# Optimization experiments

Hardware: AMD Instinct MI355X
Metric: run time of the kernel (lower is better)

## Reference

```python
import jax, jax.numpy as jnp
import numpy as np

GRID_SIZE, SPLINE_ORDER = 5, 3  # efficient-kan KANLinear defaults
NUM_BASES = GRID_SIZE + SPLINE_ORDER


def b_splines(x, grid):
    # x: (N, in_dim), grid: (in_dim, GRID_SIZE + 2*SPLINE_ORDER + 1)
    xe = x[..., None]
    bases = ((xe >= grid[:, :-1]) & (xe < grid[:, 1:])).astype(x.dtype)
    for k in range(1, SPLINE_ORDER + 1):  # Cox-de Boor recursion (static, 3 iters)
        left = (xe - grid[:, : -(k + 1)]) / (grid[:, k:-1] - grid[:, : -(k + 1)])
        right = (grid[:, k + 1:] - xe) / (grid[:, k + 1:] - grid[:, 1:-k])
        bases = left * bases[..., :-1] + right * bases[..., 1:]
    return bases  # (N, in_dim, NUM_BASES)


def kan_linear(x, grid, base_w, spline_w, scaler):
    # base branch: SiLU(x) @ W_base^T ; spline branch: B-spline basis @ scaled spline weights
    n = x.shape[0]
    out_dim = base_w.shape[0]
    base = jax.nn.silu(x) @ base_w.T
    bs = b_splines(x, grid).reshape(n, -1)                    # (N, in*NUM_BASES)
    sw = (spline_w * scaler[..., None]).reshape(out_dim, -1)  # (out, in*NUM_BASES)
    return base + bs @ sw.T


def setup_inputs() -> dict:
    key = jax.random.key(0)
    N, E, F, H, C, L = 50000, 500000, 128, 128, 40, 3
    ks = jax.random.split(key, 8)
    x = jax.random.normal(ks[0], (N, F), dtype=jnp.float32)
    edge_index = jax.random.randint(ks[1], (2, E), 0, N)
    # KAN grid (registered buffer in efficient-kan): uniform over [-1,1] extended by spline_order
    h_step = 2.0 / GRID_SIZE
    pts = np.arange(-SPLINE_ORDER, GRID_SIZE + SPLINE_ORDER + 1) * h_step - 1.0
    grid_mp = jnp.asarray(np.tile(pts, (F, 1)), dtype=jnp.float32)
    D = F + L * H  # skip-concat dim into output KANLinear
    grid_out = jnp.asarray(np.tile(pts, (D, 1)), dtype=jnp.float32)
    s = 0.1
    conv_base_w = jax.random.normal(ks[2], (L, H, F), dtype=jnp.float32) * s
    conv_spline_w = jax.random.normal(ks[3], (L, H, F, NUM_BASES), dtype=jnp.float32) * s
    conv_scaler = jnp.ones((L, H, F), dtype=jnp.float32)
    conv_bias = jnp.zeros((L, H), dtype=jnp.float32)
    bn_gamma = jnp.ones((L, H), dtype=jnp.float32)
    bn_beta = jnp.zeros((L, H), dtype=jnp.float32)
    out_base_w = jax.random.normal(ks[4], (C, D), dtype=jnp.float32) * s
    out_spline_w = jax.random.normal(ks[5], (C, D, NUM_BASES), dtype=jnp.float32) * s
    out_scaler = jnp.ones((C, D), dtype=jnp.float32)
    return dict(x=x, edge_index=edge_index, grid_mp=grid_mp, conv_base_w=conv_base_w,
                conv_spline_w=conv_spline_w, conv_scaler=conv_scaler, conv_bias=conv_bias,
                bn_gamma=bn_gamma, bn_beta=bn_beta, grid_out=grid_out,
                out_base_w=out_base_w, out_spline_w=out_spline_w, out_scaler=out_scaler)


def reference(x, edge_index, grid_mp, conv_base_w, conv_spline_w, conv_scaler, conv_bias,
              bn_gamma, bn_beta, grid_out, out_base_w, out_spline_w, out_scaler):
    N = x.shape[0]
    L = conv_base_w.shape[0]
    # GCN normalization with self-loops (computed once; identical each layer)
    loop = jnp.arange(N)
    src = jnp.concatenate([edge_index[0], loop])
    dst = jnp.concatenate([edge_index[1], loop])
    deg = jax.ops.segment_sum(jnp.ones_like(src, dtype=x.dtype), dst, num_segments=N)
    dinv = jnp.where(deg > 0, jax.lax.rsqrt(jnp.maximum(deg, 1.0)), 0.0)
    norm = dinv[src] * dinv[dst]  # (E+N,)
    feats = [x]
    for i in range(L):  # static layer loop
        h = kan_linear(x, grid_mp, conv_base_w[i], conv_spline_w[i], conv_scaler[i])
        # symmetric-normalized sparse aggregation (gather on src, scatter-add on dst)
        h = jax.ops.segment_sum(h[src] * norm[:, None], dst, num_segments=N) + conv_bias[i]
        # BatchNorm1d (training mode: biased batch statistics over nodes)
        mu = h.mean(axis=0)
        var = h.var(axis=0)
        x = (h - mu) * jax.lax.rsqrt(var + 1e-5) * bn_gamma[i] + bn_beta[i]
        feats.append(x)  # dropout p=0.0 is identity
    xc = jnp.concatenate(feats, axis=1)  # skip-concat: (N, F + L*H)
    logits = kan_linear(xc, grid_out, out_base_w, out_spline_w, out_scaler)
    return jax.nn.log_softmax(logits, axis=1)
```

## Files before the change

kernel.cpp:

```cpp
#include <hip/hip_runtime.h>
#include <hip/hip_bf16.h>
#include <math.h>

#define F_IN   128
#define HID    128
#define NLAYER 3
#define NCLS   40
#define DCAT   512
#define OOUT   64

typedef short s16x8 __attribute__((ext_vector_type(8)));
typedef unsigned short u16x8 __attribute__((ext_vector_type(8)));
typedef unsigned short u16x4 __attribute__((ext_vector_type(4)));
typedef float f32x4 __attribute__((ext_vector_type(4)));


static __device__ __forceinline__ float silu_f(float x) {
    return x / (1.f + __expf(-x));
}

static __device__ __forceinline__ unsigned short f2bf_rn(float f) {
    union { __hip_bfloat16 h; unsigned short u; } cv;
    cv.h = __float2bfloat16(f);
    return cv.u;
}

static __device__ __forceinline__ void gload_lds16(const void* g, void* l) {
    __builtin_amdgcn_global_load_lds(
        (const __attribute__((address_space(1))) void*)g,
        (__attribute__((address_space(3))) void*)l, 16, 0, 0);
}


__global__ __launch_bounds__(256) void deg_init_kernel(int* deg, int N) {
    for (int i = blockIdx.x * blockDim.x + threadIdx.x; i < N; i += gridDim.x * blockDim.x)
        deg[i] = 1;
}

__global__ __launch_bounds__(256) void deg_count_kernel(const int* __restrict__ dst, int E, int* deg) {
    for (int i = blockIdx.x * blockDim.x + threadIdx.x; i < E; i += gridDim.x * blockDim.x)
        atomicAdd(&deg[dst[i]], 1);
}

__global__ __launch_bounds__(256) void dinv_kernel(const int* __restrict__ deg, float* dinv, int N) {
    for (int i = blockIdx.x * blockDim.x + threadIdx.x; i < N; i += gridDim.x * blockDim.x)
        dinv[i] = rsqrtf((float)deg[i]);
}

__global__ __launch_bounds__(256) void scan_reduce_kernel(const int* __restrict__ deg, int* __restrict__ bsum, int N) {
    __shared__ int sh[256];
    int t = threadIdx.x;
    int e = blockIdx.x * 256 + t;
    sh[t] = (e < N) ? deg[e] : 0;
    __syncthreads();
#pragma unroll
    for (int off = 128; off > 0; off >>= 1) {
        if (t < off) sh[t] += sh[t + off];
        __syncthreads();
    }
    if (t == 0) bsum[blockIdx.x] = sh[0];
}

__global__ __launch_bounds__(256) void scan_top_kernel(const int* __restrict__ bsum, int* __restrict__ bbase, int nsb) {
    __shared__ int sh[256];
    int t = threadIdx.x;
    int chunk = (nsb + 255) >> 8;
    int begin = t * chunk;
    int end = begin + chunk; if (end > nsb) end = nsb;
    int s = 0;
    for (int i = begin; i < end; ++i) s += bsum[i];
    sh[t] = s;
    __syncthreads();
#pragma unroll
    for (int off = 1; off < 256; off <<= 1) {
        int v = 0;
        if (t >= off) v = sh[t - off];
        __syncthreads();
        if (t >= off) sh[t] += v;
        __syncthreads();
    }
    int run = (t == 0) ? 0 : sh[t - 1];
    for (int i = begin; i < end; ++i) {
        bbase[i] = run;
        run += bsum[i];
    }
}

__global__ __launch_bounds__(256) void scan_write_kernel(const int* __restrict__ deg,
                                                         const int* __restrict__ bbase,
                                                         int* __restrict__ offs, int* __restrict__ cursor, int N) {
    __shared__ int sh[256];
    int t = threadIdx.x;
    int e = blockIdx.x * 256 + t;
    int d = (e < N) ? deg[e] : 0;
    sh[t] = d;
    __syncthreads();
#pragma unroll
    for (int off = 1; off < 256; off <<= 1) {
        int v = 0;
        if (t >= off) v = sh[t - off];
        __syncthreads();
        if (t >= off) sh[t] += v;
        __syncthreads();
    }
    int incl = sh[t] + bbase[blockIdx.x];
    int excl = incl - d;
    if (e < N) {
        offs[e] = excl;
        cursor[e] = excl;
        if (e == N - 1) offs[N] = incl;
    }
}

__global__ __launch_bounds__(256) void fill_kernel(const int* __restrict__ src, const int* __restrict__ dst,
                                                   int E, int N, int* cursor, int* __restrict__ csr) {
    int total = E + N;
    for (int i = blockIdx.x * blockDim.x + threadIdx.x; i < total; i += gridDim.x * blockDim.x) {
        if (i < E) {
            int d = dst[i];
            int p = atomicAdd(&cursor[d], 1);
            csr[p] = src[i];
        } else {
            int n = i - E;
            int p = atomicAdd(&cursor[n], 1);
            csr[p] = n;
        }
    }
}

__global__ __launch_bounds__(256) void pack_conv_mfma(const float* __restrict__ bw,
                                                      const float* __restrict__ sw,
                                                      const float* __restrict__ sc,
                                                      unsigned short* __restrict__ wpk) {
    int total = NLAYER * 9 * 128 * 128;
    for (int idx = blockIdx.x * blockDim.x + threadIdx.x; idx < total; idx += gridDim.x * blockDim.x) {
        int kd = idx & 127;
        int o  = (idx >> 7) & 127;
        int cc = (idx >> 14) % 9;
        int l  = idx / (9 << 14);
        int k = kd ^ ((o & 7) << 3);
        float v;
        if (cc == 8) {
            v = bw[(l * 128 + o) * 128 + k];
        } else {
            int f = cc * 16 + (k >> 3);
            int j = k & 7;
            int base = (l * 128 + o) * 128 + f;
            v = sw[base * 8 + j] * sc[base];
        }
        wpk[idx] = f2bf_rn(v);
    }
}

__global__ __launch_bounds__(256) void pack_out_mfma(const float* __restrict__ bw,
                                                     const float* __restrict__ sw,
                                                     const float* __restrict__ sc,
                                                     unsigned short* __restrict__ wpk) {
    int total = 4 * 9 * 64 * 128;
    for (int idx = blockIdx.x * blockDim.x + threadIdx.x; idx < total; idx += gridDim.x * blockDim.x) {
        int kd = idx & 127;
        int o  = (idx >> 7) & 63;
        int cc = (idx >> 13) % 9;
        int g  = idx / (9 << 13);
        int k = kd ^ ((o & 7) << 3);
        float v = 0.f;
        if (o < NCLS) {
            if (cc == 8) {
                int f = g * 128 + k;
                v = bw[o * DCAT + f];
            } else {
                int f = g * 128 + cc * 16 + (k >> 3);
                int j = k & 7;
                int base = o * DCAT + f;
                v = sw[base * 8 + j] * sc[base];
            }
        }
        wpk[idx] = f2bf_rn(v);
    }
}


__global__ __launch_bounds__(256) void copyx_kernel(const float* __restrict__ x, float* __restrict__ xc, int N) {
    int total = N * F_IN;
    for (int idx = blockIdx.x * blockDim.x + threadIdx.x; idx < total; idx += gridDim.x * blockDim.x) {
        int n = idx >> 7, f = idx & 127;
        xc[(size_t)n * DCAT + f] = x[idx];
    }
}

__global__ __launch_bounds__(512) void affine_init_kernel(float* scA, float* shA) {
    int i = threadIdx.x;
    scA[i] = 1.f; shA[i] = 0.f;
}

template<bool CONV, bool INIT>
__global__ __launch_bounds__(256, 2) void kan_fused_kernel(
    const float* __restrict__ xc, int in_off,
    const float* __restrict__ scA, const float* __restrict__ shA,
    const unsigned short* __restrict__ wconv,
    const unsigned short* __restrict__ wout,
    unsigned short* __restrict__ silbuf,
    unsigned short* __restrict__ htmp,
    const float* __restrict__ dinv,
    float* __restrict__ out_acc, int N) {

    constexpr int LDS_WC = CONV ? 32768 : 0;
    __shared__ __align__(16) char lds[32768 + LDS_WC + 16384];
    char* lds_phi = lds;
    char* lds_wc  = lds + 32768;
    char* lds_wo  = lds + 32768 + LDS_WC;

    const int tid = threadIdx.x;
    const int lane = tid & 63;
    const int wave = tid >> 6;
    const int wr = wave >> 1, wc = wave & 1;
    const int l15 = lane & 15, lg = lane >> 4;
    const int nblk = blockIdx.x * 128;

    const float g0 = -1.f - 3.f * 0.4f;
    const float invh = 1.f / 0.4f;

    const int fg = tid & 3;
    const int n0 = tid >> 2;

    f32x4 accc[4][4];
    f32x4 acco[4][2];
    if (CONV) {
#pragma unroll
        for (int r = 0; r < 4; ++r)
#pragma unroll
            for (int c = 0; c < 4; ++c) accc[r][c] = (f32x4)0.f;
    }
#pragma unroll
    for (int r = 0; r < 4; ++r)
#pragma unroll
        for (int c = 0; c < 2; ++c) acco[r][c] = (f32x4)0.f;

    float4 xq[2], scq, shq;
    auto ldx = [&](int cc) {
        int f0 = in_off + cc * 16 + fg * 4;
        scq = *(const float4*)(scA + f0);
        shq = *(const float4*)(shA + f0);
        int gn0 = nblk + n0, gn1 = gn0 + 64;
        xq[0] = (gn0 < N) ? *(const float4*)(xc + (size_t)gn0 * DCAT + f0) : (float4){0.f,0.f,0.f,0.f};
        xq[1] = (gn1 < N) ? *(const float4*)(xc + (size_t)gn1 * DCAT + f0) : (float4){0.f,0.f,0.f,0.f};
    };

    u16x8 pcur[2][4];
    auto phi_compute = [&](int ccc) {
#pragma unroll
        for (int g2 = 0; g2 < 2; ++g2) {
            float xi[4] = {xq[g2].x, xq[g2].y, xq[g2].z, xq[g2].w};
            float scr[4] = {scq.x, scq.y, scq.z, scq.w};
            float shr[4] = {shq.x, shq.y, shq.z, shq.w};
            u16x4 sv;
#pragma unroll
            for (int fl = 0; fl < 4; ++fl) {
                float y = fmaf(xi[fl], scr[fl], shr[fl]);
                sv[fl] = f2bf_rn(silu_f(y));
                float t = (y - g0) * invh;
                float cf = floorf(t);
                int c = (int)cf;
                float u = t - cf;
                float um = 1.f - u;
                float u2 = u * u;
                float um2 = um * um;
                float w0 = um2 * um * (1.f / 6.f);
                float w3 = u2 * u * (1.f / 6.f);
                float w1 = fmaf(fmaf(0.5f, u, -1.f), u2, 2.f / 3.f);
                float w2 = fmaf(fmaf(-0.5f, u, 0.5f), u2, fmaf(0.5f, u, 1.f / 6.f));
                bool e[11];
#pragma unroll
                for (int v = 0; v < 11; ++v) e[v] = (c == v);
#pragma unroll
                for (int s = 0; s < 8; ++s) {
                    float val = 0.f;
                    val = e[s] ? w3 : val;
                    val = e[s + 1] ? w2 : val;
                    val = e[s + 2] ? w1 : val;
                    val = e[s + 3] ? w0 : val;
                    pcur[g2][fl][s] = f2bf_rn(val);
                }
            }
            int gn = nblk + n0 + g2 * 64;
            if (gn < N) {
                int fdst = (ccc * 16 + fg * 4) ^ ((n0 & 7) << 3);
                *(u16x4*)(silbuf + (size_t)gn * 128 + fdst) = sv;
            }
        }
    };

    auto stage_w = [&](int cc) {
        if (CONV) {
            const unsigned short* wcsrc = wconv + (size_t)cc * 128 * 128;
#pragma unroll
            for (int i = 0; i < 8; ++i) {
                int e = tid + i * 256;
                gload_lds16(wcsrc + e * 8, lds_wc + e * 16);
            }
        }
        const unsigned short* wosrc = wout + (size_t)cc * 64 * 128;
#pragma unroll
        for (int i = 0; i < 4; ++i) {
            int e = tid + i * 256;
            gload_lds16(wosrc + e * 8, lds_wo + e * 16);
        }
    };

    auto mfma_phase = [&]() {
#pragma unroll
        for (int kk = 0; kk < 4; ++kk) {
            const int kb = kk * 64 + lg * 16;
            s16x8 af[4];
#pragma unroll
            for (int r = 0; r < 4; ++r) {
                int n = wr * 64 + r * 16 + l15;
                af[r] = *(const s16x8*)(lds_phi + n * 256 + (kb ^ ((n & 7) << 4)));
            }
            if (CONV) {
#pragma unroll
                for (int c = 0; c < 4; ++c) {
                    int o = wc * 64 + c * 16 + l15;
                    s16x8 b = *(const s16x8*)(lds_wc + o * 256 + (kb ^ ((o & 7) << 4)));
#pragma unroll
                    for (int r = 0; r < 4; ++r)
                        accc[r][c] = __builtin_amdgcn_mfma_f32_16x16x32_bf16(af[r], b, accc[r][c], 0, 0, 0);
                }
            }
#pragma unroll
            for (int c = 0; c < 2; ++c) {
                int o = wc * 32 + c * 16 + l15;
                s16x8 b = *(const s16x8*)(lds_wo + o * 256 + (kb ^ ((o & 7) << 4)));
#pragma unroll
                for (int r = 0; r < 4; ++r)
                    acco[r][c] = __builtin_amdgcn_mfma_f32_16x16x32_bf16(af[r], b, acco[r][c], 0, 0, 0);
            }
        }
    };

    ldx(0);
    phi_compute(0);

    for (int cc = 0; cc < 8; ++cc) {
        __syncthreads();
        stage_w(cc);
#pragma unroll
        for (int g2 = 0; g2 < 2; ++g2) {
            int n = n0 + g2 * 64;
            int swz = (n & 7) << 4;
#pragma unroll
            for (int i = 0; i < 4; ++i) {
                int byte = n * 256 + ((fg * 64 + i * 16) ^ swz);
                *(u16x8*)(lds_phi + byte) = pcur[g2][i];
            }
        }
        __syncthreads();
        if (cc < 7) ldx(cc + 1);
        mfma_phase();
        if (cc < 7) phi_compute(cc + 1);
    }

    __syncthreads();
    stage_w(8);
    {
        const unsigned short* ssrc = silbuf + (size_t)nblk * 128;
#pragma unroll
        for (int i = 0; i < 8; ++i) {
            int e = tid + i * 256;
            gload_lds16(ssrc + e * 8, lds_phi + e * 16);
        }
    }
    __syncthreads();
    mfma_phase();

#pragma unroll
    for (int r = 0; r < 4; ++r) {
        int nb = nblk + wr * 64 + r * 16 + lg * 4;
        if (CONV) {
#pragma unroll
            for (int c = 0; c < 4; ++c) {
                int o = wc * 64 + c * 16 + l15;
#pragma unroll
                for (int q = 0; q < 4; ++q) {
                    int n = nb + q;
                    if (n < N) htmp[(size_t)n * HID + o] = f2bf_rn(accc[r][c][q] * dinv[n]);
                }
            }
        }
#pragma unroll
        for (int c = 0; c < 2; ++c) {
            int o = wc * 32 + c * 16 + l15;
#pragma unroll
            for (int q = 0; q < 4; ++q) {
                int n = nb + q;
                if (n < N) {
                    size_t a = (size_t)n * OOUT + o;
                    float v = acco[r][c][q];
                    if (!INIT) v += out_acc[a];
                    out_acc[a] = v;
                }
            }
        }
    }
}

__global__ __launch_bounds__(256) void agg_kernel(const unsigned short* __restrict__ h,
                                                  const float* __restrict__ dinv,
                                                  const int* __restrict__ offs,
                                                  const int* __restrict__ csr,
                                                  const float* __restrict__ bias,
                                                  float* __restrict__ xc, int out_off, int N) {
    int n = blockIdx.x * 4 + (threadIdx.x >> 6);
    if (n >= N) return;
    int lane = threadIdx.x & 63;
    int s = offs[n], e = offs[n + 1];
    float a0 = 0.f, a1 = 0.f, b0 = 0.f, b1 = 0.f;
    float c0 = 0.f, c1 = 0.f, d0 = 0.f, d1 = 0.f;
    int i = s;
    for (; i + 4 <= e; i += 4) {
        int v0 = csr[i], v1 = csr[i + 1], v2 = csr[i + 2], v3 = csr[i + 3];
        unsigned u0 = *(const unsigned*)(h + (size_t)v0 * HID + lane * 2);
        unsigned u1 = *(const unsigned*)(h + (size_t)v1 * HID + lane * 2);
        unsigned u2 = *(const unsigned*)(h + (size_t)v2 * HID + lane * 2);
        unsigned u3 = *(const unsigned*)(h + (size_t)v3 * HID + lane * 2);
        a0 += __uint_as_float(u0 << 16);
        a1 += __uint_as_float(u0 & 0xffff0000u);
        b0 += __uint_as_float(u1 << 16);
        b1 += __uint_as_float(u1 & 0xffff0000u);
        c0 += __uint_as_float(u2 << 16);
        c1 += __uint_as_float(u2 & 0xffff0000u);
        d0 += __uint_as_float(u3 << 16);
        d1 += __uint_as_float(u3 & 0xffff0000u);
    }
    for (; i < e; ++i) {
        int v = csr[i];
        unsigned u = *(const unsigned*)(h + (size_t)v * HID + lane * 2);
        a0 += __uint_as_float(u << 16);
        a1 += __uint_as_float(u & 0xffff0000u);
    }
    a0 += b0 + c0 + d0;
    a1 += b1 + c1 + d1;
    float dn = dinv[n];
    float2 bv = *(const float2*)(bias + lane * 2);
    float2 res = {fmaf(a0, dn, bv.x), fmaf(a1, dn, bv.y)};
    *(float2*)(xc + (size_t)n * DCAT + out_off + lane * 2) = res;
}

__global__ __launch_bounds__(128) void bn_stats_kernel(const float* __restrict__ xc, int off, int N,
                                                       float* __restrict__ bnsum, float* __restrict__ bnsq) {
    int f = threadIdx.x;
    float s = 0.f, q = 0.f;
    for (int n = blockIdx.x; n < N; n += gridDim.x) {
        float v = xc[(size_t)n * DCAT + off + f];
        s += v;
        q += v * v;
    }
    atomicAdd(&bnsum[f], s);
    atomicAdd(&bnsq[f], q);
}

__global__ __launch_bounds__(128) void bn_affine_kernel(const float* __restrict__ bnsum,
                                                        const float* __restrict__ bnsq,
                                                        const float* __restrict__ gamma,
                                                        const float* __restrict__ beta,
                                                        float* scA, float* shA, int seg_off, float invN) {
    int f = threadIdx.x;
    float mu = bnsum[f] * invN;
    float var = bnsq[f] * invN - mu * mu;
    float rs = rsqrtf(var + 1e-5f);
    float s = gamma[f] * rs;
    scA[seg_off + f] = s;
    shA[seg_off + f] = fmaf(-mu, s, beta[f]);
}

__global__ __launch_bounds__(256) void logsoftmax_kernel(const float* __restrict__ oacc,
                                                         float* __restrict__ out, int N) {
    for (int n = blockIdx.x * blockDim.x + threadIdx.x; n < N; n += gridDim.x * blockDim.x) {
        const float* row = oacc + (size_t)n * OOUT;
        float m = -1e30f;
#pragma unroll
        for (int j = 0; j < NCLS; ++j) m = fmaxf(m, row[j]);
        float s = 0.f;
#pragma unroll
        for (int j = 0; j < NCLS; ++j) s += __expf(row[j] - m);
        float lse = m + __logf(s);
        float* orow = out + (size_t)n * NCLS;
#pragma unroll
        for (int j = 0; j < NCLS; ++j) orow[j] = row[j] - lse;
    }
}


extern "C" void kernel_launch(void* const* d_in, const int* in_sizes, int n_in,
                              void* d_out, int out_size, void* d_ws, size_t ws_size,
                              hipStream_t stream) {
    const float* x            = (const float*)d_in[0];
    const int*   eidx         = (const int*)d_in[1];
    const float* conv_base_w  = (const float*)d_in[3];
    const float* conv_spline_w= (const float*)d_in[4];
    const float* conv_scaler  = (const float*)d_in[5];
    const float* conv_bias    = (const float*)d_in[6];
    const float* bn_gamma     = (const float*)d_in[7];
    const float* bn_beta      = (const float*)d_in[8];
    const float* out_base_w   = (const float*)d_in[10];
    const float* out_spline_w = (const float*)d_in[11];
    const float* out_scaler   = (const float*)d_in[12];
    float* out = (float*)d_out;

    int N = in_sizes[0] / F_IN;
    int E = in_sizes[1] / 2;
    const int* esrc = eidx;
    const int* edst = eidx + E;

    int blocks = (N + 127) / 128;
    int npad = blocks * 128;
    int nsb = (N + 255) / 256;

    char* p = (char*)d_ws;
    auto carve = [&](size_t bytes) {
        char* r = p;
        p += (bytes + 255) & ~(size_t)255;
        return r;
    };
    float* xc   = (float*)carve((size_t)N * DCAT * 4);
    unsigned short* htmp = (unsigned short*)carve((size_t)npad * HID * 2);
    float* oacc = (float*)carve((size_t)npad * OOUT * 4);
    unsigned short* silbuf = (unsigned short*)carve((size_t)npad * 128 * 2);
    float* dinv = (float*)carve((size_t)N * 4);
    float* bn   = (float*)carve((size_t)NLAYER * 2 * HID * 4);
    float* scA  = (float*)carve((size_t)DCAT * 4);
    float* shA  = (float*)carve((size_t)DCAT * 4);
    unsigned short* wpkc = (unsigned short*)carve((size_t)NLAYER * 9 * 128 * 128 * 2);
    unsigned short* wpko = (unsigned short*)carve((size_t)4 * 9 * 64 * 128 * 2);
    int* deg    = (int*)carve((size_t)N * 4);
    int* offs   = (int*)carve((size_t)(N + 1) * 4);
    int* cursor = (int*)carve((size_t)(N + 1) * 4);
    int* bsum   = (int*)carve((size_t)nsb * 4);
    int* bbase  = (int*)carve((size_t)nsb * 4);
    int* csr    = (int*)carve((size_t)(E + N) * 4);

    hipMemsetAsync(bn, 0, NLAYER * 2 * HID * 4, stream);

    deg_init_kernel<<<512, 256, 0, stream>>>(deg, N);
    deg_count_kernel<<<1024, 256, 0, stream>>>(edst, E, deg);
    dinv_kernel<<<512, 256, 0, stream>>>(deg, dinv, N);
    scan_reduce_kernel<<<nsb, 256, 0, stream>>>(deg, bsum, N);
    scan_top_kernel<<<1, 256, 0, stream>>>(bsum, bbase, nsb);
    scan_write_kernel<<<nsb, 256, 0, stream>>>(deg, bbase, offs, cursor, N);
    fill_kernel<<<1024, 256, 0, stream>>>(esrc, edst, E, N, cursor, csr);

    pack_conv_mfma<<<1024, 256, 0, stream>>>(conv_base_w, conv_spline_w, conv_scaler, wpkc);
    pack_out_mfma<<<1024, 256, 0, stream>>>(out_base_w, out_spline_w, out_scaler, wpko);
    copyx_kernel<<<2048, 256, 0, stream>>>(x, xc, N);
    affine_init_kernel<<<1, 512, 0, stream>>>(scA, shA);

    float invN = 1.f / (float)N;
    for (int l = 0; l < NLAYER; ++l) {
        int in_off = l * HID;
        int out_off = (l + 1) * HID;
        const unsigned short* wl = wpkc + (size_t)l * 9 * 128 * 128;
        const unsigned short* wo = wpko + (size_t)l * 9 * 64 * 128;
        if (l == 0)
            kan_fused_kernel<true, true><<<blocks, 256, 0, stream>>>(
                xc, in_off, scA, shA, wl, wo, silbuf, htmp, dinv, oacc, N);
        else
            kan_fused_kernel<true, false><<<blocks, 256, 0, stream>>>(
                xc, in_off, scA, shA, wl, wo, silbuf, htmp, dinv, oacc, N);
        agg_kernel<<<(N + 3) / 4, 256, 0, stream>>>(htmp, dinv, offs, csr, conv_bias + l * HID, xc, out_off, N);
        float* bnsum = bn + l * 2 * HID;
        float* bnsq  = bnsum + HID;
        bn_stats_kernel<<<256, 128, 0, stream>>>(xc, out_off, N, bnsum, bnsq);
        bn_affine_kernel<<<1, 128, 0, stream>>>(bnsum, bnsq, bn_gamma + l * HID, bn_beta + l * HID,
                                                scA, shA, out_off, invN);
    }

    kan_fused_kernel<false, false><<<blocks, 256, 0, stream>>>(
        xc, 384, scA, shA, nullptr, wpko + (size_t)3 * 9 * 64 * 128, silbuf, nullptr, dinv, oacc, N);

    logsoftmax_kernel<<<(N + 255) / 256, 256, 0, stream>>>(oacc, out, N);
}
```

Baseline: 561.5 us.

## Pre-pack weights in MFMA fragment order and load B operands directly from global

The weight packers now write conv and output KAN weights in per-lane MFMA B-fragment order, so each lane reads one contiguous 16-byte vector straight from global memory (L2/L1) instead of staging weight tiles into LDS. This removes the weight LDS staging, the swizzled LDS reads, and their LDS footprint (48KB down to 32KB per block), which may allow more resident blocks. The cost is that every wave re-reads weights from cache inside the MFMA loop, exposing global load latency with no prefetch.

```diff
diff --git a/kernel.cpp b/kernel.cpp
--- a/kernel.cpp
+++ b/kernel.cpp
@@ -132,13 +132,16 @@
                                                       const float* __restrict__ sw,
                                                       const float* __restrict__ sc,
                                                       unsigned short* __restrict__ wpk) {
-    int total = NLAYER * 9 * 128 * 128;
+    int total = NLAYER * 9 * 4 * 8 * 64 * 8;
     for (int idx = blockIdx.x * blockDim.x + threadIdx.x; idx < total; idx += gridDim.x * blockDim.x) {
-        int kd = idx & 127;
-        int o  = (idx >> 7) & 127;
-        int cc = (idx >> 14) % 9;
-        int l  = idx / (9 << 14);
-        int k = kd ^ ((o & 7) << 3);
+        int e    = idx & 7;
+        int lane = (idx >> 3) & 63;
+        int cf   = (idx >> 9) & 7;
+        int kk   = (idx >> 12) & 3;
+        int cc   = (idx >> 14) % 9;
+        int l    = idx / (9 << 14);
+        int o = cf * 16 + (lane & 15);
+        int k = kk * 32 + ((lane >> 4) << 3) + e;
         float v;
         if (cc == 8) {
             v = bw[(l * 128 + o) * 128 + k];
@@ -156,13 +159,16 @@
                                                      const float* __restrict__ sw,
                                                      const float* __restrict__ sc,
                                                      unsigned short* __restrict__ wpk) {
-    int total = 4 * 9 * 64 * 128;
+    int total = 36 * 4 * 4 * 64 * 8;
     for (int idx = blockIdx.x * blockDim.x + threadIdx.x; idx < total; idx += gridDim.x * blockDim.x) {
-        int kd = idx & 127;
-        int o  = (idx >> 7) & 63;
-        int cc = (idx >> 13) % 9;
-        int g  = idx / (9 << 13);
-        int k = kd ^ ((o & 7) << 3);
+        int e    = idx & 7;
+        int lane = (idx >> 3) & 63;
+        int cf   = (idx >> 9) & 3;
+        int kk   = (idx >> 11) & 3;
+        int gcc  = idx >> 13;
+        int g = gcc / 9, cc = gcc % 9;
+        int o = cf * 16 + (lane & 15);
+        int k = kk * 32 + ((lane >> 4) << 3) + e;
         float v = 0.f;
         if (o < NCLS) {
             if (cc == 8) {
@@ -204,11 +210,7 @@
     const float* __restrict__ dinv,
     float* __restrict__ out_acc, int N) {
 
-    constexpr int LDS_WC = CONV ? 32768 : 0;
-    __shared__ __align__(16) char lds[32768 + LDS_WC + 16384];
-    char* lds_phi = lds;
-    char* lds_wc  = lds + 32768;
-    char* lds_wo  = lds + 32768 + LDS_WC;
+    __shared__ __align__(16) char lds_phi[32768];
 
     const int tid = threadIdx.x;
     const int lane = tid & 63;
@@ -290,24 +292,7 @@
         }
     };
 
-    auto stage_w = [&](int cc) {
-        if (CONV) {
-            const unsigned short* wcsrc = wconv + (size_t)cc * 128 * 128;
-#pragma unroll
-            for (int i = 0; i < 8; ++i) {
-                int e = tid + i * 256;
-                gload_lds16(wcsrc + e * 8, lds_wc + e * 16);
-            }
-        }
-        const unsigned short* wosrc = wout + (size_t)cc * 64 * 128;
-#pragma unroll
-        for (int i = 0; i < 4; ++i) {
-            int e = tid + i * 256;
-            gload_lds16(wosrc + e * 8, lds_wo + e * 16);
-        }
-    };
-
-    auto mfma_phase = [&]() {
+    auto mfma_phase = [&](const unsigned short* wcb, const unsigned short* wob) {
 #pragma unroll
         for (int kk = 0; kk < 4; ++kk) {
             const int kb = kk * 64 + lg * 16;
@@ -320,8 +305,8 @@
             if (CONV) {
 #pragma unroll
                 for (int c = 0; c < 4; ++c) {
-                    int o = wc * 64 + c * 16 + l15;
-                    s16x8 b = *(const s16x8*)(lds_wc + o * 256 + (kb ^ ((o & 7) << 4)));
+                    int cf = wc * 4 + c;
+                    s16x8 b = *(const s16x8*)(wcb + (((size_t)kk * 8 + cf) * 64 + lane) * 8);
 #pragma unroll
                     for (int r = 0; r < 4; ++r)
                         accc[r][c] = __builtin_amdgcn_mfma_f32_16x16x32_bf16(af[r], b, accc[r][c], 0, 0, 0);
@@ -329,8 +314,8 @@
             }
 #pragma unroll
             for (int c = 0; c < 2; ++c) {
-                int o = wc * 32 + c * 16 + l15;
-                s16x8 b = *(const s16x8*)(lds_wo + o * 256 + (kb ^ ((o & 7) << 4)));
+                int cf = wc * 2 + c;
+                s16x8 b = *(const s16x8*)(wob + (((size_t)kk * 4 + cf) * 64 + lane) * 8);
 #pragma unroll
                 for (int r = 0; r < 4; ++r)
                     acco[r][c] = __builtin_amdgcn_mfma_f32_16x16x32_bf16(af[r], b, acco[r][c], 0, 0, 0);
@@ -343,7 +328,6 @@
 
     for (int cc = 0; cc < 8; ++cc) {
         __syncthreads();
-        stage_w(cc);
 #pragma unroll
         for (int g2 = 0; g2 < 2; ++g2) {
             int n = n0 + g2 * 64;
@@ -356,12 +340,11 @@
         }
         __syncthreads();
         if (cc < 7) ldx(cc + 1);
-        mfma_phase();
+        mfma_phase(CONV ? wconv + (size_t)cc * 16384 : nullptr, wout + (size_t)cc * 8192);
         if (cc < 7) phi_compute(cc + 1);
     }
 
     __syncthreads();
-    stage_w(8);
     {
         const unsigned short* ssrc = silbuf + (size_t)nblk * 128;
 #pragma unroll
@@ -371,7 +354,7 @@
         }
     }
     __syncthreads();
-    mfma_phase();
+    mfma_phase(CONV ? wconv + (size_t)8 * 16384 : nullptr, wout + (size_t)8 * 8192);
 
 #pragma unroll
     for (int r = 0; r < 4; ++r) {
@@ -531,7 +514,7 @@
     float* scA  = (float*)carve((size_t)DCAT * 4);
     float* shA  = (float*)carve((size_t)DCAT * 4);
     unsigned short* wpkc = (unsigned short*)carve((size_t)NLAYER * 9 * 128 * 128 * 2);
-    unsigned short* wpko = (unsigned short*)carve((size_t)4 * 9 * 64 * 128 * 2);
+    unsigned short* wpko = (unsigned short*)carve((size_t)36 * 64 * 128 * 2);
     int* deg    = (int*)carve((size_t)N * 4);
     int* offs   = (int*)carve((size_t)(N + 1) * 4);
     int* cursor = (int*)carve((size_t)(N + 1) * 4);
@@ -558,8 +541,8 @@
     for (int l = 0; l < NLAYER; ++l) {
         int in_off = l * HID;
         int out_off = (l + 1) * HID;
-        const unsigned short* wl = wpkc + (size_t)l * 9 * 128 * 128;
-        const unsigned short* wo = wpko + (size_t)l * 9 * 64 * 128;
+        const unsigned short* wl = wpkc + (size_t)l * 9 * 16384;
+        const unsigned short* wo = wpko + (size_t)l * 9 * 8192;
         if (l == 0)
             kan_fused_kernel<true, true><<<blocks, 256, 0, stream>>>(
                 xc, in_off, scA, shA, wl, wo, silbuf, htmp, dinv, oacc, N);
@@ -575,7 +558,7 @@
     }
 
     kan_fused_kernel<false, false><<<blocks, 256, 0, stream>>>(
-        xc, 384, scA, shA, nullptr, wpko + (size_t)3 * 9 * 64 * 128, silbuf, nullptr, dinv, oacc, N);
+        xc, 384, scA, shA, nullptr, wpko + (size_t)3 * 9 * 8192, silbuf, nullptr, dinv, oacc, N);
 
     logsoftmax_kernel<<<(N + 255) / 256, 256, 0, stream>>>(oacc, out, N);
 }
```

New measurement: 648.0 us. 15.4% more time.
